# Performance work log

Hardware: AMD Instinct MI355X
Metric: run time of the kernel (lower is better)

The kernel has to match this reference:

```python
import jax, jax.numpy as jnp
import numpy as np

CHUNK = 32


def l2norm(x):
    return x * jax.lax.rsqrt(jnp.sum(x * x, -1, keepdims=True) + 1e-6)


def causal_dwconv(x, w):
    # x: (b, l, C), w: (C, 1, k) -- depthwise causal 1D conv (left pad k-1)
    k = w.shape[-1]
    xt = jnp.transpose(x, (0, 2, 1))
    xt = jnp.pad(xt, ((0, 0), (0, 0), (k - 1, 0)))
    y = jax.lax.conv_general_dilated(xt, w, (1,), 'VALID',
                                     dimension_numbers=('NCH', 'OIH', 'NCH'),
                                     feature_group_count=xt.shape[1])
    return jnp.transpose(y, (0, 2, 1))


def delta_rule_chunkwise(q, k, v, beta):
    # q,k: (b,h,L,dk), v: (b,h,L,dv), beta: (b,h,L). L must be divisible by CHUNK.
    b, h, L, dk = q.shape
    dv = v.shape[-1]
    n = L // CHUNK
    q = l2norm(q)
    k = l2norm(k)
    v = v * beta[..., None]
    kb = k * beta[..., None]
    resh = lambda t: t.reshape(b, h, n, CHUNK, t.shape[-1])
    q, k, v, kb = (resh(t) for t in (q, k, v, kb))
    strict = jnp.tril(jnp.ones((CHUNK, CHUNK), bool), -1)
    A = jnp.where(strict, -(kb @ jnp.swapaxes(k, -1, -2)), 0.0)
    eye = jnp.eye(CHUNK, dtype=A.dtype)
    # UT transform: the sequential forward-substitution loop computes T = (I - A)^{-1}
    T = jax.scipy.linalg.solve_triangular(eye - A, jnp.broadcast_to(eye, A.shape), lower=True)
    u = T @ v
    w = T @ kb
    incl = jnp.tril(jnp.ones((CHUNK, CHUNK), bool))  # lower incl. diag

    def step(S, xs):
        q_i, k_i, u_i, w_i = xs
        attn = jnp.where(incl, q_i @ jnp.swapaxes(k_i, -1, -2), 0.0)
        u_hat = u_i - w_i @ S
        o_i = q_i @ S + attn @ u_hat
        return S + jnp.swapaxes(k_i, -1, -2) @ u_hat, o_i

    xs = tuple(jnp.moveaxis(t, 2, 0) for t in (q, k, u, w))
    S0 = jnp.zeros((b, h, dk, dv), q.dtype)
    S, o = jax.lax.scan(step, S0, xs)
    o = jnp.moveaxis(o, 0, 2).reshape(b, h, L, dv)
    return o, S


def branch_stats(x):
    # per-head stats over the feature dim: mean, std(ddof=1), mean|x|, L2 norm
    m = jnp.mean(x, -1, keepdims=True)
    s = jnp.std(x, -1, keepdims=True, ddof=1)
    a = jnp.mean(jnp.abs(x), -1, keepdims=True)
    l = jnp.sqrt(jnp.sum(x * x, -1, keepdims=True))
    return jnp.concatenate([m, s, a, l], -1)


def reference(hidden_states, q_w, k_w, v_w, b_w, qc_w, kc_w, vc_w,
              fir_w1, fir_w3, fir_w7, fir_w31,
              mlp_w1, mlp_b1, mlp_w2, mlp_b2, gate_log_temp, onorm_w, o_w):
    B, L, D = hidden_states.shape
    H = gate_log_temp.shape[0]
    dk = q_w.shape[1] // H
    dv = v_w.shape[1] // H
    # projections + causal short conv + silu
    q = jax.nn.silu(causal_dwconv(hidden_states @ q_w, qc_w))
    k = jax.nn.silu(causal_dwconv(hidden_states @ k_w, kc_w))
    v = jax.nn.silu(causal_dwconv(hidden_states @ v_w, vc_w))
    q = q.reshape(B, L, H, dk)
    k = k.reshape(B, L, H, dk)
    v_direct = v.reshape(B, L, H, dv)
    beta = jax.nn.sigmoid(hidden_states @ b_w)  # (B,L,H)
    delta_out, _ = delta_rule_chunkwise(
        jnp.transpose(q, (0, 2, 1, 3)), jnp.transpose(k, (0, 2, 1, 3)),
        jnp.transpose(v_direct, (0, 2, 1, 3)), jnp.transpose(beta, (0, 2, 1)))
    delta_out = jnp.transpose(delta_out, (0, 2, 1, 3))  # (B,L,H,dv)
    # multi-scale depthwise FIR branches on v
    v_flat = v_direct.reshape(B, L, H * dv)
    firs = [causal_dwconv(v_flat, w).reshape(B, L, H, dv)
            for w in (fir_w1, fir_w3, fir_w7, fir_w31)]
    branches = firs + [delta_out, v_direct]  # num_streams = 6
    S = len(branches)
    stats = jnp.concatenate([branch_stats(x) for x in branches], -1)  # (B,L,H,S*4)
    gate_in = jnp.concatenate([hidden_states, stats.reshape(B, L, H * S * 4)], -1)
    hgate = jax.nn.gelu(gate_in @ mlp_w1 + mlp_b1, approximate=False)
    logits = (hgate @ mlp_w2 + mlp_b2).reshape(B, L, H, S)
    temp = jax.nn.softplus(gate_log_temp) + 0.5  # min_gate_temp = 0.5
    weights = jax.nn.softmax(logits / temp[None, None, :, None], axis=-1)
    fused = sum(weights[..., i, None] * br for i, br in enumerate(branches))
    # RMSNorm over head_v_dim (eps=1e-5)
    fused = fused * jax.lax.rsqrt(jnp.mean(fused * fused, -1, keepdims=True) + 1e-5) * onorm_w
    return fused.reshape(B, L, H * dv) @ o_w


def setup_inputs() -> dict:
    key = jax.random.key(0)
    B, L, D, H = 2, 2048, 1024, 4
    dk = dv = D // H
    S = 6
    ks = iter(jax.random.split(key, 32))
    nrm = lambda shape, s=0.02: jax.random.normal(next(ks), shape, jnp.float32) * s

    def fir(kw):
        # delta init (last tap = 1) plus small noise
        base = jnp.zeros((H * dv, 1, kw), jnp.float32).at[:, 0, -1].set(1.0)
        return base + nrm((H * dv, 1, kw))

    gate_in_dim = D + S * 4 * H  # 1120
    hgd = D * 2 // 2             # 1024
    b2 = np.zeros(H * S, np.float32)
    for h in range(H):
        b2[h * S + S - 1] = 2.0  # value_bias_init on direct-value stream
    return {
        'hidden_states': jax.random.normal(next(ks), (B, L, D), jnp.float32),
        'q_w': nrm((D, D)), 'k_w': nrm((D, D)), 'v_w': nrm((D, D)),
        'b_w': nrm((D, H)),
        'qc_w': nrm((D, 1, 4), 0.3), 'kc_w': nrm((D, 1, 4), 0.3), 'vc_w': nrm((D, 1, 4), 0.3),
        'fir_w1': fir(1), 'fir_w3': fir(3), 'fir_w7': fir(7), 'fir_w31': fir(31),
        'mlp_w1': nrm((gate_in_dim, hgd)), 'mlp_b1': jnp.zeros((hgd,), jnp.float32),
        'mlp_w2': nrm((hgd, H * S)), 'mlp_b2': jnp.asarray(b2),
        'gate_log_temp': jnp.zeros((H,), jnp.float32),
        'onorm_w': jnp.ones((dv,), jnp.float32),
        'o_w': nrm((D, D)),
    }
```

## Files before the change

kernel.cpp:

```cpp
#include <hip/hip_runtime.h>
#include <hip/hip_bf16.h>
#include <math.h>

#define B_ 2
#define L_ 2048
#define D_ 1024
#define H_ 4
#define NC 64

typedef unsigned short ushort_t;
typedef __bf16 bf16x8 __attribute__((ext_vector_type(8)));
typedef float f32x4 __attribute__((ext_vector_type(4)));
typedef ushort_t u16x8 __attribute__((ext_vector_type(8)));

__device__ __forceinline__ ushort_t f2bs(float f) {
    __hip_bfloat16 h = __float2bfloat16(f);
    ushort_t u;
    __builtin_memcpy(&u, &h, 2);
    return u;
}

__device__ __forceinline__ float wred(float v) {
    v += __shfl_down(v, 32);
    v += __shfl_down(v, 16);
    v += __shfl_down(v, 8);
    v += __shfl_down(v, 4);
    v += __shfl_down(v, 2);
    v += __shfl_down(v, 1);
    return v;
}

__device__ __forceinline__ void gload16(const void* g, void* l) {
    __builtin_amdgcn_global_load_lds((const __attribute__((address_space(1))) void*)g,
                                     (__attribute__((address_space(3))) void*)l, 16, 0, 0);
}

#define LGKM0_BAR()                                          \
    do {                                                     \
        asm volatile("s_waitcnt lgkmcnt(0)" ::: "memory");   \
        __builtin_amdgcn_s_barrier();                        \
    } while (0)

__global__ __launch_bounds__(256) void tcast_k(const float* __restrict__ W,
                                               ushort_t* __restrict__ WT, int K, int N) {
    __shared__ float tile[32 * 33];
    const int k0 = blockIdx.y << 5, n0 = blockIdx.x << 5;
    for (int e = threadIdx.x; e < 1024; e += 256)
        tile[(e >> 5) * 33 + (e & 31)] = W[(size_t)(k0 + (e >> 5)) * N + n0 + (e & 31)];
    __syncthreads();
    for (int e = threadIdx.x; e < 1024; e += 256)
        WT[(size_t)(n0 + (e >> 5)) * K + k0 + (e & 31)] = f2bs(tile[(e & 31) * 33 + (e >> 5)]);
}

__global__ __launch_bounds__(256) void cast_k(const float* __restrict__ x,
                                              ushort_t* __restrict__ y) {
    const int i = blockIdx.x * 256 + threadIdx.x;
    const float4 v = *(const float4*)&x[(size_t)i * 4];
    ushort4 p;
    p.x = f2bs(v.x); p.y = f2bs(v.y); p.z = f2bs(v.z); p.w = f2bs(v.w);
    *(ushort4*)&y[(size_t)i * 4] = p;
}

template <int ACT>
__global__ __launch_bounds__(256) void gemm_bf(const ushort_t* __restrict__ A,
                                               const ushort_t* __restrict__ Bt,
                                               const float* __restrict__ bias,
                                               float* __restrict__ C,
                                               int M, int N, int K) {
    __shared__ ushort_t As[128 * 32];
    __shared__ ushort_t Bs[128 * 32];
    const int t = threadIdx.x;
    const int wv = t >> 6, l = t & 63;
    const int m0 = blockIdx.y << 7, n0 = blockIdx.x << 7;
    const int wm = wv & 1, wn = wv >> 1;
    const int q4 = l >> 4, c16 = l & 15;
    f32x4 acc[4][4];
#pragma unroll
    for (int i = 0; i < 4; ++i)
#pragma unroll
        for (int j = 0; j < 4; ++j) {
            f32x4 z = {0.f, 0.f, 0.f, 0.f};
            acc[i][j] = z;
        }
    const int srow = (l >> 2);
    const int scol = (l & 3) << 3;
    for (int k0 = 0; k0 < K; k0 += 32) {
        __syncthreads();
#pragma unroll
        for (int si = 0; si < 2; ++si) {
            const int s = wv * 2 + si;
            gload16(&A[(size_t)(m0 + s * 16 + srow) * K + k0 + scol], &As[s * 512]);
            gload16(&Bt[(size_t)(n0 + s * 16 + srow) * K + k0 + scol], &Bs[s * 512]);
        }
        __syncthreads();
        bf16x8 af[4], bff[4];
#pragma unroll
        for (int mi = 0; mi < 4; ++mi)
            af[mi] = *(const bf16x8*)&As[(wm * 64 + mi * 16 + c16) * 32 + q4 * 8];
#pragma unroll
        for (int ni = 0; ni < 4; ++ni)
            bff[ni] = *(const bf16x8*)&Bs[(wn * 64 + ni * 16 + c16) * 32 + q4 * 8];
#pragma unroll
        for (int mi = 0; mi < 4; ++mi)
#pragma unroll
            for (int ni = 0; ni < 4; ++ni)
                acc[mi][ni] = __builtin_amdgcn_mfma_f32_16x16x32_bf16(af[mi], bff[ni],
                                                                     acc[mi][ni], 0, 0, 0);
    }
#pragma unroll
    for (int mi = 0; mi < 4; ++mi)
#pragma unroll
        for (int ni = 0; ni < 4; ++ni)
#pragma unroll
            for (int r = 0; r < 4; ++r) {
                const int row = m0 + wm * 64 + mi * 16 + q4 * 4 + r;
                const int col = n0 + wn * 64 + ni * 16 + c16;
                float v = acc[mi][ni][r];
                if (ACT == 1) {
                    v += bias[col];
                    v = 0.5f * v * (1.0f + erff(v * 0.70710678118654752f));
                }
                C[(size_t)row * N + col] = v;
            }
}

template <int DO_NORM, int EMIT_F32, int EMIT_BF>
__global__ __launch_bounds__(256) void convql_k(const float* __restrict__ X,
                                                const float* __restrict__ cw,
                                                float* __restrict__ Y,
                                                ushort_t* __restrict__ Ybf) {
    __shared__ float xs[35 * 256];
    const int bid = blockIdx.x;
    const int h = bid & 3, lt = (bid >> 2) & 63, b = bid >> 8;
    const int t = threadIdx.x;
    const int l0 = lt << 5;
    const int cg = (h << 8) | t;
    for (int e = t; e < 35 * 256; e += 256) {
        const int r = e >> 8, c = e & 255;
        const int gl = l0 + r - 3;
        xs[e] = (gl >= 0) ? X[((size_t)(b * L_) + gl) * 3072 + (h << 8) + c] : 0.f;
    }
    const float w0 = cw[cg * 4 + 0], w1 = cw[cg * 4 + 1];
    const float w2 = cw[cg * 4 + 2], w3 = cw[cg * 4 + 3];
    __syncthreads();
    float yr[32];
#pragma unroll
    for (int l = 0; l < 32; ++l) {
        const float a = xs[(l + 0) * 256 + t] * w0 + xs[(l + 1) * 256 + t] * w1 +
                        xs[(l + 2) * 256 + t] * w2 + xs[(l + 3) * 256 + t] * w3;
        yr[l] = a / (1.f + expf(-a));
    }
    if (DO_NORM) {
        __syncthreads();
#pragma unroll
        for (int l = 0; l < 32; ++l) xs[l * 256 + t] = yr[l];
        __syncthreads();
        const int wv = t >> 6, lane = t & 63;
#pragma unroll
        for (int ri = 0; ri < 8; ++ri) {
            const int r = wv * 8 + ri;
            float4 v = *(float4*)&xs[r * 256 + lane * 4];
            float ss = v.x * v.x + v.y * v.y + v.z * v.z + v.w * v.w;
            ss = wred(ss);
            ss = __shfl(ss, 0);
            const float s = rsqrtf(ss + 1e-6f);
            v.x *= s; v.y *= s; v.z *= s; v.w *= s;
            const size_t go = ((size_t)(b * L_) + l0 + r) * 1024 + (h << 8) + lane * 4;
            if (EMIT_F32) *(float4*)&Y[go] = v;
            if (EMIT_BF) {
                ushort4 p;
                p.x = f2bs(v.x); p.y = f2bs(v.y); p.z = f2bs(v.z); p.w = f2bs(v.w);
                *(ushort4*)&Ybf[go] = p;
            }
        }
    } else {
#pragma unroll
        for (int l = 0; l < 32; ++l)
            if (EMIT_F32) Y[((size_t)(b * L_) + l0 + l) * 1024 + cg] = yr[l];
    }
}

__global__ __launch_bounds__(256) void fir_k(const float* __restrict__ V,
                                             const float* __restrict__ w1w,
                                             const float* __restrict__ w3w,
                                             const float* __restrict__ w7w,
                                             const float* __restrict__ w31w,
                                             float* __restrict__ o1,
                                             float* __restrict__ o3,
                                             float* __restrict__ o7,
                                             float* __restrict__ o31) {
    __shared__ float xs[62 * 256];
    const int bid = blockIdx.x;
    const int h = bid & 3, lt = (bid >> 2) & 63, b = bid >> 8;
    const int t = threadIdx.x;
    const int l0 = lt << 5;
    const int cg = (h << 8) | t;
    for (int e = t; e < 62 * 256; e += 256) {
        const int r = e >> 8, c = e & 255;
        const int gl = l0 + r - 30;
        xs[e] = (gl >= 0) ? V[((size_t)(b * L_) + gl) * 1024 + (h << 8) + c] : 0.f;
    }
    float lw31[31], lw7[7], lw3[3];
#pragma unroll
    for (int j = 0; j < 31; ++j) lw31[j] = w31w[cg * 31 + j];
#pragma unroll
    for (int j = 0; j < 7; ++j) lw7[j] = w7w[cg * 7 + j];
#pragma unroll
    for (int j = 0; j < 3; ++j) lw3[j] = w3w[cg * 3 + j];
    const float lw1 = w1w[cg];
    __syncthreads();
    for (int l = 0; l < 32; ++l) {
        float a31 = 0.f, a7 = 0.f, a3 = 0.f, v = 0.f;
#pragma unroll
        for (int j = 0; j < 31; ++j) {
            v = xs[(l + j) * 256 + t];
            a31 += v * lw31[j];
            if (j >= 24) a7 += v * lw7[j - 24];
            if (j >= 28) a3 += v * lw3[j - 28];
        }
        const size_t go = ((size_t)(b * L_) + l0 + l) * 1024 + cg;
        o31[go] = a31;
        o7[go] = a7;
        o3[go] = a3;
        o1[go] = v * lw1;
    }
}

__global__ __launch_bounds__(64) void beta_k(const float* __restrict__ hs,
                                             const float* __restrict__ bw,
                                             float* __restrict__ beta,
                                             ushort_t* __restrict__ gin) {
    const int row = blockIdx.x;
    const int lane = threadIdx.x;
    float a0 = 0, a1 = 0, a2 = 0, a3 = 0;
    const float* hp = hs + (size_t)row * D_;
    ushort_t* gp = gin + (size_t)row * 1120;
    for (int c = lane; c < D_; c += 64) {
        const float x = hp[c];
        gp[c] = f2bs(x);
        a0 += x * bw[c * 4 + 0];
        a1 += x * bw[c * 4 + 1];
        a2 += x * bw[c * 4 + 2];
        a3 += x * bw[c * 4 + 3];
    }
    a0 = wred(a0); a1 = wred(a1); a2 = wred(a2); a3 = wred(a3);
    if (lane == 0) {
        float* o = beta + (size_t)row * 4;
        o[0] = 1.f / (1.f + expf(-a0));
        o[1] = 1.f / (1.f + expf(-a1));
        o[2] = 1.f / (1.f + expf(-a2));
        o[3] = 1.f / (1.f + expf(-a3));
    }
}

__global__ __launch_bounds__(256) void prep2_k(const ushort_t* __restrict__ qbf,
                                               const ushort_t* __restrict__ kbf,
                                               const float* __restrict__ vg,
                                               const float* __restrict__ beta,
                                               ushort_t* __restrict__ wbf,
                                               float* __restrict__ ub,
                                               ushort_t* __restrict__ atg,
                                               ushort_t* __restrict__ ktg) {
    __shared__ ushort_t k_lds[32 * 264];
    __shared__ ushort_t kT_lds[256 * 32];
    __shared__ ushort_t vT_lds[256 * 32];
    __shared__ float Am[32 * 33];
    __shared__ float Tm[32 * 33];
    __shared__ ushort_t Tb[32 * 40];
    __shared__ float beta_s[32];
    const int bid = blockIdx.x;
    const int bh = bid >> 6, ci = bid & 63;
    const int b = bh >> 2, h = bh & 3;
    const int t = threadIdx.x;
    const int wv = t >> 6, lane = t & 63;
    const int l16 = lane & 15, quad = lane >> 4;
    const size_t cb = (size_t)bid;
    const size_t grow = ((size_t)(b * L_ + ci * 32)) * 1024 + (h << 8);
    const f32x4 z4 = {0.f, 0.f, 0.f, 0.f};

    if (t < 32) beta_s[t] = beta[(size_t)(b * L_ + ci * 32 + t) * 4 + h];
#pragma unroll
    for (int j = 0; j < 4; ++j) {
        const int idx = j * 2048 + t * 8, r = idx >> 8, c = idx & 255;
        *(u16x8*)&k_lds[r * 264 + c] = *(const u16x8*)&kbf[grow + (size_t)r * 1024 + c];
    }
#pragma unroll
    for (int j = 0; j < 8; ++j) {
        const int e = j * 1024 + t * 4, r = e >> 8, c = e & 255;
        const float4 v4 = *(const float4*)&vg[grow + (size_t)r * 1024 + c];
        const float vv[4] = {v4.x, v4.y, v4.z, v4.w};
#pragma unroll
        for (int x = 0; x < 4; ++x) {
            const int cc = c + x;
            const int sp = (r >> 3) ^ ((cc >> 1) & 3);
            vT_lds[cc * 32 + sp * 8 + (r & 7)] = f2bs(vv[x]);
        }
    }
    const int mi = wv & 1, ni = wv >> 1;
    f32x4 g = z4, atv = z4;
#pragma unroll
    for (int s = 0; s < 8; ++s) {
        const bf16x8 a =
            *(const bf16x8*)&kbf[grow + (size_t)(mi * 16 + l16) * 1024 + s * 32 + (quad << 3)];
        const bf16x8 bb =
            *(const bf16x8*)&kbf[grow + (size_t)(ni * 16 + l16) * 1024 + s * 32 + (quad << 3)];
        const bf16x8 qa =
            *(const bf16x8*)&qbf[grow + (size_t)(mi * 16 + l16) * 1024 + s * 32 + (quad << 3)];
        g = __builtin_amdgcn_mfma_f32_16x16x32_bf16(a, bb, g, 0, 0, 0);
        atv = __builtin_amdgcn_mfma_f32_16x16x32_bf16(qa, bb, atv, 0, 0, 0);
    }
    __syncthreads();
#pragma unroll
    for (int r = 0; r < 4; ++r) {
        const int row = mi * 16 + (quad << 2) + r;
        const int col = ni * 16 + l16;
        Am[row * 33 + col] = (col < row) ? -beta_s[row] * g[r] : 0.f;
        Tm[row * 33 + col] = (row == col) ? 1.f : 0.f;
        atg[cb * 1024 + row * 32 + col] = (col <= row) ? f2bs(atv[r]) : (ushort_t)0;
    }
#pragma unroll
    for (int j = 0; j < 8; ++j) {
        const int e = j * 1024 + t * 4, r = e >> 8, c = e & 255;
#pragma unroll
        for (int x = 0; x < 4; ++x) {
            const int cc = c + x;
            const int sp = (r >> 3) ^ ((cc >> 1) & 3);
            kT_lds[cc * 32 + sp * 8 + (r & 7)] = k_lds[r * 264 + cc];
        }
    }
    __syncthreads();
    for (int i = 1; i < 32; ++i) {
        if (t < 32) {
            float s = 0.f;
            for (int j = 0; j < i; ++j) s += Am[i * 33 + j] * Tm[j * 33 + t];
            Tm[i * 33 + t] += s;
        }
        __syncthreads();
    }
#pragma unroll
    for (int j = 0; j < 4; ++j) {
        const int e = j * 256 + t, i = e >> 5, jj = e & 31;
        Tb[i * 40 + jj] = f2bs(Tm[i * 33 + jj] * beta_s[jj]);
    }
    __syncthreads();
    const bf16x8 tf = *(const bf16x8*)&Tb[(mi * 16 + l16) * 40 + (quad << 3)];
#pragma unroll
    for (int j = 0; j < 8; ++j) {
        const int nt = ni * 8 + j;
        const int d = (nt << 4) + l16;
        const int sp = quad ^ ((d >> 1) & 3);
        const bf16x8 kb = *(const bf16x8*)&kT_lds[d * 32 + (sp << 3)];
        const bf16x8 vb = *(const bf16x8*)&vT_lds[d * 32 + (sp << 3)];
        const f32x4 wacc = __builtin_amdgcn_mfma_f32_16x16x32_bf16(tf, kb, z4, 0, 0, 0);
        const f32x4 uacc = __builtin_amdgcn_mfma_f32_16x16x32_bf16(tf, vb, z4, 0, 0, 0);
#pragma unroll
        for (int r = 0; r < 4; ++r) {
            const int row = mi * 16 + (quad << 2) + r;
            wbf[cb * 8192 + row * 256 + d] = f2bs(wacc[r]);
            ub[cb * 8192 + (size_t)row * 256 + d] = uacc[r];
        }
    }
#pragma unroll
    for (int j = 0; j < 4; ++j) {
        const int idx = j * 2048 + t * 8;
        const int c = idx >> 5, sl = (idx & 31) >> 3;
        const int sp = sl ^ ((c >> 1) & 3);
        *(u16x8*)&ktg[cb * 8192 + c * 32 + sl * 8] = *(const u16x8*)&kT_lds[c * 32 + sp * 8];
    }
}

__global__ __launch_bounds__(256, 1) void scan4_k(const ushort_t* __restrict__ qbf,
                                                  const ushort_t* __restrict__ wbf,
                                                  const float* __restrict__ ubuf,
                                                  const ushort_t* __restrict__ atg,
                                                  const ushort_t* __restrict__ ktg,
                                                  float* __restrict__ dlt) {
    __shared__ ushort_t uh_lds[16 * 40];
    __shared__ ushort_t S_lds[16 * 264];
    const int t = threadIdx.x;
    const int wv = t >> 6, lane = t & 63;
    const int bh = blockIdx.x & 7, tile = blockIdx.x >> 3;
    const int b = bh >> 2, h = bh & 3;
    const int l16 = lane & 15, quad = lane >> 4;
    for (int e = t; e < 16 * 264; e += 256) S_lds[e] = 0;

    f32x4 Sacc[8];
#pragma unroll
    for (int j = 0; j < 8; ++j) {
        f32x4 z = {0.f, 0.f, 0.f, 0.f};
        Sacc[j] = z;
    }

    bf16x8 wfA[8], qfA[8], atfA, ktA[8];
    bf16x8 wfB[8], qfB[8], atfB, ktB[8];
    float uvA[4], uvB[4];

    auto loadf = [&](int ci, bf16x8* wf, bf16x8* qf, bf16x8& atf, float* uv, bf16x8* ktf) {
        const size_t cb = (size_t)(bh * NC + ci);
        if (wv < 2) {
            const ushort_t* wsrc = wbf + cb * 8192;
            const ushort_t* qsrc = qbf + ((size_t)(b * L_ + ci * 32)) * 1024 + (h << 8);
            const int i = (wv << 4) + l16;
#pragma unroll
            for (int s = 0; s < 8; ++s) {
                wf[s] = *(const bf16x8*)&wsrc[i * 256 + s * 32 + (quad << 3)];
                qf[s] = *(const bf16x8*)&qsrc[(size_t)i * 1024 + s * 32 + (quad << 3)];
            }
            atf = *(const bf16x8*)&atg[cb * 1024 + i * 32 + (quad << 3)];
#pragma unroll
            for (int r = 0; r < 4; ++r)
                uv[r] = ubuf[cb * 8192 + (size_t)((wv << 4) + (quad << 2) + r) * 256 +
                             (tile << 4) + l16];
        } else {
            const ushort_t* ksrc = ktg + cb * 8192;
#pragma unroll
            for (int j = 0; j < 8; ++j) {
                const int c = ((((wv - 2) << 3) + j) << 4) + l16;
                ktf[j] = *(const bf16x8*)&ksrc[c * 32 + (quad << 3)];
            }
        }
    };
    auto sfrag = [&](int k0) -> bf16x8 {
        return *(const bf16x8*)&S_lds[l16 * 264 + k0 + (quad << 3)];
    };
    auto uhfrag = [&]() -> bf16x8 {
        return *(const bf16x8*)&uh_lds[l16 * 40 + (quad << 3)];
    };
    auto compute = [&](int ci, bf16x8* wf, bf16x8* qf, bf16x8& atf, float* uv, bf16x8* ktf) {
        const size_t gbase = ((size_t)(b * L_ + ci * 32)) * D_ + (h << 8);
        if (wv < 2) {
            f32x4 acc = {0.f, 0.f, 0.f, 0.f};
#pragma unroll
            for (int s = 0; s < 8; ++s)
                acc = __builtin_amdgcn_mfma_f32_16x16x32_bf16(wf[s], sfrag(s * 32), acc, 0, 0, 0);
            ushort4 up;
            up.x = f2bs(uv[0] - acc[0]);
            up.y = f2bs(uv[1] - acc[1]);
            up.z = f2bs(uv[2] - acc[2]);
            up.w = f2bs(uv[3] - acc[3]);
            *(ushort4*)&uh_lds[l16 * 40 + (wv << 4) + (quad << 2)] = up;
        }
        LGKM0_BAR();
        if (wv < 2) {
            f32x4 o = {0.f, 0.f, 0.f, 0.f};
#pragma unroll
            for (int s = 0; s < 8; ++s)
                o = __builtin_amdgcn_mfma_f32_16x16x32_bf16(qf[s], sfrag(s * 32), o, 0, 0, 0);
            o = __builtin_amdgcn_mfma_f32_16x16x32_bf16(atf, uhfrag(), o, 0, 0, 0);
#pragma unroll
            for (int r = 0; r < 4; ++r)
                dlt[gbase + (size_t)((wv << 4) + (quad << 2) + r) * D_ + (tile << 4) + l16] =
                    o[r];
        } else {
            const bf16x8 uf = uhfrag();
#pragma unroll
            for (int j = 0; j < 8; ++j)
                Sacc[j] = __builtin_amdgcn_mfma_f32_16x16x32_bf16(ktf[j], uf, Sacc[j], 0, 0, 0);
        }
        LGKM0_BAR();
        if (wv >= 2) {
#pragma unroll
            for (int j = 0; j < 8; ++j) {
                const int c0 = ((((wv - 2) << 3) + j) << 4) + (quad << 2);
#pragma unroll
                for (int r = 0; r < 4; ++r)
                    S_lds[l16 * 264 + c0 + r] = f2bs(Sacc[j][r]);
            }
        }
        LGKM0_BAR();
    };

    loadf(0, wfA, qfA, atfA, uvA, ktA);
    LGKM0_BAR();
    for (int ci = 0; ci < NC; ci += 2) {
        loadf(ci + 1, wfB, qfB, atfB, uvB, ktB);
        compute(ci, wfA, qfA, atfA, uvA, ktA);
        if (ci + 2 < NC) loadf(ci + 2, wfA, qfA, atfA, uvA, ktA);
        compute(ci + 1, wfB, qfB, atfB, uvB, ktB);
    }
}

__global__ __launch_bounds__(64) void stats_k(const float* __restrict__ f1,
                                              const float* __restrict__ f3,
                                              const float* __restrict__ f7,
                                              const float* __restrict__ f31,
                                              const float* __restrict__ dl,
                                              const float* __restrict__ vv,
                                              ushort_t* __restrict__ gin) {
    const int row = blockIdx.x;
    const int lane = threadIdx.x;
    const float* ptrs[6] = {f1, f3, f7, f31, dl, vv};
    const size_t base = (size_t)row * 256;
    ushort_t* gp = gin + (size_t)(row >> 2) * 1120 + 1024 + (row & 3) * 24;
    for (int br = 0; br < 6; ++br) {
        const float4 x = *(const float4*)&ptrs[br][base + lane * 4];
        float s1 = x.x + x.y + x.z + x.w;
        float s2 = x.x * x.x + x.y * x.y + x.z * x.z + x.w * x.w;
        float sa = fabsf(x.x) + fabsf(x.y) + fabsf(x.z) + fabsf(x.w);
        s1 = wred(s1); s2 = wred(s2); sa = wred(sa);
        if (lane == 0) {
            const float m = s1 / 256.f;
            float var = (s2 - 256.f * m * m) / 255.f;
            if (var < 0.f) var = 0.f;
            gp[br * 4 + 0] = f2bs(m);
            gp[br * 4 + 1] = f2bs(sqrtf(var));
            gp[br * 4 + 2] = f2bs(sa / 256.f);
            gp[br * 4 + 3] = f2bs(sqrtf(s2));
        }
    }
}

__global__ __launch_bounds__(256) void wts_k(const float* __restrict__ hg,
                                             const float* __restrict__ w2,
                                             const float* __restrict__ b2,
                                             const float* __restrict__ glt,
                                             float* __restrict__ wts) {
    const int row = blockIdx.x;
    const int h = threadIdx.x >> 6, lane = threadIdx.x & 63;
    float hv[16];
    const float* hp = hg + (size_t)row * 1024;
#pragma unroll
    for (int ii = 0; ii < 16; ++ii) hv[ii] = hp[lane + 64 * ii];
    float lg[6];
#pragma unroll
    for (int s = 0; s < 6; ++s) {
        const int j = h * 6 + s;
        float acc = 0.f;
#pragma unroll
        for (int ii = 0; ii < 16; ++ii) acc += hv[ii] * w2[(size_t)(lane + 64 * ii) * 24 + j];
        lg[s] = wred(acc);
    }
    if (lane == 0) {
        const float temp = log1pf(expf(glt[h])) + 0.5f;
        float mx = -1e30f;
#pragma unroll
        for (int s = 0; s < 6; ++s) {
            lg[s] = (lg[s] + b2[h * 6 + s]) / temp;
            mx = fmaxf(mx, lg[s]);
        }
        float se = 0.f;
#pragma unroll
        for (int s = 0; s < 6; ++s) {
            lg[s] = expf(lg[s] - mx);
            se += lg[s];
        }
        float* o = &wts[(size_t)row * 24 + h * 6];
        const float inv = 1.f / se;
#pragma unroll
        for (int s = 0; s < 6; ++s) o[s] = lg[s] * inv;
    }
}

__global__ __launch_bounds__(1024) void fuse_k(const float* __restrict__ f1,
                                               const float* __restrict__ f3,
                                               const float* __restrict__ f7,
                                               const float* __restrict__ f31,
                                               const float* __restrict__ dl,
                                               const float* __restrict__ vv,
                                               const float* __restrict__ wts,
                                               const float* __restrict__ onw,
                                               ushort_t* __restrict__ fused) {
    __shared__ float wloc[24];
    __shared__ float psum[16];
    const int row = blockIdx.x, t = threadIdx.x;
    if (t < 24) wloc[t] = wts[(size_t)row * 24 + t];
    __syncthreads();
    const int h = t >> 8, dd = t & 255;
    const size_t idx = (size_t)row * 1024 + t;
    const float* ptrs[6] = {f1, f3, f7, f31, dl, vv};
    float f = 0.f;
#pragma unroll
    for (int br = 0; br < 6; ++br) f += wloc[h * 6 + br] * ptrs[br][idx];
    float ss = wred(f * f);
    const int wave = t >> 6;
    if ((t & 63) == 0) psum[wave] = ss;
    __syncthreads();
    const float tot = psum[h * 4 + 0] + psum[h * 4 + 1] + psum[h * 4 + 2] + psum[h * 4 + 3];
    const float scale = rsqrtf(tot / 256.f + 1e-5f);
    fused[idx] = f2bs(f * scale * onw[dd]);
}

extern "C" void kernel_launch(void* const* d_in, const int* in_sizes, int n_in,
                              void* d_out, int out_size, void* d_ws, size_t ws_size,
                              hipStream_t stream) {
    const float* hs   = (const float*)d_in[0];
    const float* q_w  = (const float*)d_in[1];
    const float* k_w  = (const float*)d_in[2];
    const float* v_w  = (const float*)d_in[3];
    const float* b_w  = (const float*)d_in[4];
    const float* qc_w = (const float*)d_in[5];
    const float* kc_w = (const float*)d_in[6];
    const float* vc_w = (const float*)d_in[7];
    const float* f1w  = (const float*)d_in[8];
    const float* f3w  = (const float*)d_in[9];
    const float* f7w  = (const float*)d_in[10];
    const float* f31w = (const float*)d_in[11];
    const float* w1   = (const float*)d_in[12];
    const float* b1   = (const float*)d_in[13];
    const float* w2   = (const float*)d_in[14];
    const float* b2   = (const float*)d_in[15];
    const float* glt  = (const float*)d_in[16];
    const float* onw  = (const float*)d_in[17];
    const float* o_w  = (const float*)d_in[18];
    float* out = (float*)d_out;

    const size_t SZ = (size_t)B_ * L_ * D_;
    float* qlin = (float*)d_ws;
    float* klin = qlin + SZ;
    float* vlin = klin + SZ;
    float* qbuf = vlin + SZ;
    float* kbuf = qbuf + SZ;
    float* vbuf = kbuf + SZ;
    float* f31b = vbuf + SZ;
    float* wb   = f31b + SZ;
    float* ub   = wb + SZ;
    float* dlt  = ub + SZ;
    float* beta = dlt + SZ;
    float* attn = beta + (size_t)B_ * L_ * H_;
    float* stat = attn + (size_t)B_ * H_ * NC * 1024;
    float* wts  = stat + (size_t)B_ * L_ * H_ * 24;
    float* f1b = qlin;
    float* f3b = klin;
    float* f7b = vlin;
    float* hgate = kbuf;
    float* qkv = qlin;

    ushort_t* hs_bf = (ushort_t*)dlt;
    ushort_t* qwT = (ushort_t*)f31b;
    ushort_t* kwT = (ushort_t*)f31b + 1048576;
    ushort_t* vwT = (ushort_t*)f31b + 2097152;
    ushort_t* qbf = (ushort_t*)f31b + 3145728;
    ushort_t* kbf = (ushort_t*)kbuf;
    ushort_t* gin_bf = (ushort_t*)qbuf;
    ushort_t* w1T = (ushort_t*)(wb + 2359296);
    ushort_t* owT = (ushort_t*)ub;
    ushort_t* fused_bf = (ushort_t*)kbuf;
    ushort_t* ktg = (ushort_t*)klin;
    ushort_t* wbf = (ushort_t*)wb;
    ushort_t* at_bf = (ushort_t*)attn;
    (void)stat;

    const int M = B_ * L_;

    tcast_k<<<dim3(32, 32), 256, 0, stream>>>(q_w, qwT, 1024, 1024);
    tcast_k<<<dim3(32, 32), 256, 0, stream>>>(k_w, kwT, 1024, 1024);
    tcast_k<<<dim3(32, 32), 256, 0, stream>>>(v_w, vwT, 1024, 1024);
    cast_k<<<4096, 256, 0, stream>>>(hs, hs_bf);
    gemm_bf<0><<<dim3(24, 32), 256, 0, stream>>>(hs_bf, qwT, nullptr, qkv, M, 3072, 1024);
    beta_k<<<M, 64, 0, stream>>>(hs, b_w, beta, gin_bf);
    convql_k<1, 0, 1><<<512, 256, 0, stream>>>(qkv + 0,    qc_w, nullptr, qbf);
    convql_k<1, 0, 1><<<512, 256, 0, stream>>>(qkv + 1024, kc_w, nullptr, kbf);
    convql_k<0, 1, 0><<<512, 256, 0, stream>>>(qkv + 2048, vc_w, vbuf, nullptr);
    prep2_k<<<B_ * H_ * NC, 256, 0, stream>>>(qbf, kbf, vbuf, beta, wbf, ub, at_bf, ktg);
    scan4_k<<<128, 256, 0, stream>>>(qbf, wbf, ub, at_bf, ktg, dlt);
    fir_k<<<512, 256, 0, stream>>>(vbuf, f1w, f3w, f7w, f31w, f1b, f3b, f7b, f31b);
    stats_k<<<M * H_, 64, 0, stream>>>(f1b, f3b, f7b, f31b, dlt, vbuf, gin_bf);
    tcast_k<<<dim3(32, 35), 256, 0, stream>>>(w1, w1T, 1120, 1024);
    gemm_bf<1><<<dim3(8, 32), 256, 0, stream>>>(gin_bf, w1T, b1, hgate, M, 1024, 1120);
    wts_k<<<M, 256, 0, stream>>>(hgate, w2, b2, glt, wts);
    fuse_k<<<M, 1024, 0, stream>>>(f1b, f3b, f7b, f31b, dlt, vbuf, wts, onw, fused_bf);
    tcast_k<<<dim3(32, 32), 256, 0, stream>>>(o_w, owT, 1024, 1024);
    gemm_bf<0><<<dim3(8, 32), 256, 0, stream>>>(fused_bf, owT, nullptr, out, M, 1024, 1024);
}
```

Baseline: 591.6 us.

## Store scan operands in MFMA fragment order and double-buffer S in LDS

```diff
diff --git a/kernel.cpp b/kernel.cpp
--- a/kernel.cpp
+++ b/kernel.cpp
@@ -257,22 +257,25 @@
                                                const ushort_t* __restrict__ kbf,
                                                const float* __restrict__ vg,
                                                const float* __restrict__ beta,
-                                               ushort_t* __restrict__ wbf,
-                                               float* __restrict__ ub,
-                                               ushort_t* __restrict__ atg,
-                                               ushort_t* __restrict__ ktg) {
+                                               ushort_t* __restrict__ qfr,
+                                               ushort_t* __restrict__ wfr,
+                                               float* __restrict__ ufr,
+                                               ushort_t* __restrict__ atfr,
+                                               ushort_t* __restrict__ ktfr) {
     __shared__ ushort_t k_lds[32 * 264];
     __shared__ ushort_t kT_lds[256 * 32];
     __shared__ ushort_t vT_lds[256 * 32];
     __shared__ float Am[32 * 33];
     __shared__ float Tm[32 * 33];
     __shared__ ushort_t Tb[32 * 40];
+    __shared__ ushort_t at_s[32 * 40];
     __shared__ float beta_s[32];
     const int bid = blockIdx.x;
     const int bh = bid >> 6, ci = bid & 63;
     const int b = bh >> 2, h = bh & 3;
     const int t = threadIdx.x;
     const int wv = t >> 6, lane = t & 63;
+    const int mi = wv & 1, ni = wv >> 1;
     const int l16 = lane & 15, quad = lane >> 4;
     const size_t cb = (size_t)bid;
     const size_t grow = ((size_t)(b * L_ + ci * 32)) * 1024 + (h << 8);
@@ -296,7 +299,6 @@
             vT_lds[cc * 32 + sp * 8 + (r & 7)] = f2bs(vv[x]);
         }
     }
-    const int mi = wv & 1, ni = wv >> 1;
     f32x4 g = z4, atv = z4;
 #pragma unroll
     for (int s = 0; s < 8; ++s) {
@@ -308,6 +310,7 @@
             *(const bf16x8*)&qbf[grow + (size_t)(mi * 16 + l16) * 1024 + s * 32 + (quad << 3)];
         g = __builtin_amdgcn_mfma_f32_16x16x32_bf16(a, bb, g, 0, 0, 0);
         atv = __builtin_amdgcn_mfma_f32_16x16x32_bf16(qa, bb, atv, 0, 0, 0);
+        if (ni == 0) *(bf16x8*)&qfr[((cb * 2 + mi) * 8 + s) * 512 + lane * 8] = qa;
     }
     __syncthreads();
 #pragma unroll
@@ -316,7 +319,7 @@
         const int col = ni * 16 + l16;
         Am[row * 33 + col] = (col < row) ? -beta_s[row] * g[r] : 0.f;
         Tm[row * 33 + col] = (row == col) ? 1.f : 0.f;
-        atg[cb * 1024 + row * 32 + col] = (col <= row) ? f2bs(atv[r]) : (ushort_t)0;
+        at_s[row * 40 + col] = (col <= row) ? f2bs(atv[r]) : (ushort_t)0;
     }
 #pragma unroll
     for (int j = 0; j < 8; ++j) {
@@ -329,6 +332,17 @@
         }
     }
     __syncthreads();
+    if (wv < 2) {
+        const u16x8 av = *(const u16x8*)&at_s[(wv * 16 + l16) * 40 + (quad << 3)];
+        *(u16x8*)&atfr[(cb * 2 + wv) * 512 + lane * 8] = av;
+    }
+#pragma unroll
+    for (int j2 = 0; j2 < 4; ++j2) {
+        const int tc = wv * 4 + j2;
+        const int c = tc * 16 + l16;
+        const int sp = quad ^ ((c >> 1) & 3);
+        *(u16x8*)&ktfr[(cb * 16 + tc) * 512 + lane * 8] = *(const u16x8*)&kT_lds[c * 32 + sp * 8];
+    }
     for (int i = 1; i < 32; ++i) {
         if (t < 32) {
             float s = 0.f;
@@ -353,36 +367,38 @@
         const bf16x8 vb = *(const bf16x8*)&vT_lds[d * 32 + (sp << 3)];
         const f32x4 wacc = __builtin_amdgcn_mfma_f32_16x16x32_bf16(tf, kb, z4, 0, 0, 0);
         const f32x4 uacc = __builtin_amdgcn_mfma_f32_16x16x32_bf16(tf, vb, z4, 0, 0, 0);
+        *(float4*)&ufr[((cb * 16 + nt) * 2 + mi) * 256 + lane * 4] =
+            make_float4(uacc[0], uacc[1], uacc[2], uacc[3]);
 #pragma unroll
         for (int r = 0; r < 4; ++r) {
             const int row = mi * 16 + (quad << 2) + r;
-            wbf[cb * 8192 + row * 256 + d] = f2bs(wacc[r]);
-            ub[cb * 8192 + (size_t)row * 256 + d] = uacc[r];
-        }
-    }
-#pragma unroll
-    for (int j = 0; j < 4; ++j) {
-        const int idx = j * 2048 + t * 8;
-        const int c = idx >> 5, sl = (idx & 31) >> 3;
-        const int sp = sl ^ ((c >> 1) & 3);
-        *(u16x8*)&ktg[cb * 8192 + c * 32 + sl * 8] = *(const u16x8*)&kT_lds[c * 32 + sp * 8];
-    }
-}
-
-__global__ __launch_bounds__(256, 1) void scan4_k(const ushort_t* __restrict__ qbf,
-                                                  const ushort_t* __restrict__ wbf,
-                                                  const float* __restrict__ ubuf,
-                                                  const ushort_t* __restrict__ atg,
-                                                  const ushort_t* __restrict__ ktg,
+            k_lds[row * 264 + d] = f2bs(wacc[r]);
+        }
+    }
+    __syncthreads();
+    if (wv < 2) {
+#pragma unroll
+        for (int s = 0; s < 8; ++s) {
+            const u16x8 wv8 = *(const u16x8*)&k_lds[(wv * 16 + l16) * 264 + s * 32 + (quad << 3)];
+            *(u16x8*)&wfr[((cb * 2 + wv) * 8 + s) * 512 + lane * 8] = wv8;
+        }
+    }
+}
+
+__global__ __launch_bounds__(256, 1) void scan5_k(const ushort_t* __restrict__ qfr,
+                                                  const ushort_t* __restrict__ wfr,
+                                                  const float* __restrict__ ufr,
+                                                  const ushort_t* __restrict__ atfr,
+                                                  const ushort_t* __restrict__ ktfr,
                                                   float* __restrict__ dlt) {
     __shared__ ushort_t uh_lds[16 * 40];
-    __shared__ ushort_t S_lds[16 * 264];
+    __shared__ ushort_t S_lds[2][16 * 264];
     const int t = threadIdx.x;
     const int wv = t >> 6, lane = t & 63;
     const int bh = blockIdx.x & 7, tile = blockIdx.x >> 3;
     const int b = bh >> 2, h = bh & 3;
     const int l16 = lane & 15, quad = lane >> 4;
-    for (int e = t; e < 16 * 264; e += 256) S_lds[e] = 0;
+    for (int e = t; e < 16 * 264; e += 256) S_lds[0][e] = 0;
 
     f32x4 Sacc[8];
 #pragma unroll
@@ -398,73 +414,77 @@
     auto loadf = [&](int ci, bf16x8* wf, bf16x8* qf, bf16x8& atf, float* uv, bf16x8* ktf) {
         const size_t cb = (size_t)(bh * NC + ci);
         if (wv < 2) {
-            const ushort_t* wsrc = wbf + cb * 8192;
-            const ushort_t* qsrc = qbf + ((size_t)(b * L_ + ci * 32)) * 1024 + (h << 8);
-            const int i = (wv << 4) + l16;
+            const ushort_t* wsrc = wfr + (cb * 2 + wv) * 8 * 512;
+            const ushort_t* qsrc = qfr + (cb * 2 + wv) * 8 * 512;
 #pragma unroll
             for (int s = 0; s < 8; ++s) {
-                wf[s] = *(const bf16x8*)&wsrc[i * 256 + s * 32 + (quad << 3)];
-                qf[s] = *(const bf16x8*)&qsrc[(size_t)i * 1024 + s * 32 + (quad << 3)];
+                wf[s] = *(const bf16x8*)&wsrc[s * 512 + lane * 8];
+                qf[s] = *(const bf16x8*)&qsrc[s * 512 + lane * 8];
             }
-            atf = *(const bf16x8*)&atg[cb * 1024 + i * 32 + (quad << 3)];
-#pragma unroll
-            for (int r = 0; r < 4; ++r)
-                uv[r] = ubuf[cb * 8192 + (size_t)((wv << 4) + (quad << 2) + r) * 256 +
-                             (tile << 4) + l16];
+            atf = *(const bf16x8*)&atfr[(cb * 2 + wv) * 512 + lane * 8];
+            const float4 u4 = *(const float4*)&ufr[((cb * 16 + tile) * 2 + wv) * 256 + lane * 4];
+            uv[0] = u4.x; uv[1] = u4.y; uv[2] = u4.z; uv[3] = u4.w;
         } else {
-            const ushort_t* ksrc = ktg + cb * 8192;
+            const ushort_t* ksrc = ktfr + cb * 16 * 512;
 #pragma unroll
             for (int j = 0; j < 8; ++j) {
-                const int c = ((((wv - 2) << 3) + j) << 4) + l16;
-                ktf[j] = *(const bf16x8*)&ksrc[c * 32 + (quad << 3)];
+                const int tc = ((wv - 2) << 3) + j;
+                ktf[j] = *(const bf16x8*)&ksrc[tc * 512 + lane * 8];
             }
         }
     };
-    auto sfrag = [&](int k0) -> bf16x8 {
-        return *(const bf16x8*)&S_lds[l16 * 264 + k0 + (quad << 3)];
+    auto sfrag = [&](int p, int k0) -> bf16x8 {
+        return *(const bf16x8*)&S_lds[p][l16 * 264 + k0 + (quad << 3)];
     };
     auto uhfrag = [&]() -> bf16x8 {
         return *(const bf16x8*)&uh_lds[l16 * 40 + (quad << 3)];
     };
     auto compute = [&](int ci, bf16x8* wf, bf16x8* qf, bf16x8& atf, float* uv, bf16x8* ktf) {
+        const int p = ci & 1;
         const size_t gbase = ((size_t)(b * L_ + ci * 32)) * D_ + (h << 8);
         if (wv < 2) {
-            f32x4 acc = {0.f, 0.f, 0.f, 0.f};
-#pragma unroll
-            for (int s = 0; s < 8; ++s)
-                acc = __builtin_amdgcn_mfma_f32_16x16x32_bf16(wf[s], sfrag(s * 32), acc, 0, 0, 0);
+            f32x4 a0 = {0.f, 0.f, 0.f, 0.f}, a1 = {0.f, 0.f, 0.f, 0.f};
+#pragma unroll
+            for (int s = 0; s < 8; s += 2) {
+                a0 = __builtin_amdgcn_mfma_f32_16x16x32_bf16(wf[s], sfrag(p, s * 32), a0, 0, 0, 0);
+                a1 = __builtin_amdgcn_mfma_f32_16x16x32_bf16(wf[s + 1], sfrag(p, s * 32 + 32), a1,
+                                                             0, 0, 0);
+            }
             ushort4 up;
-            up.x = f2bs(uv[0] - acc[0]);
-            up.y = f2bs(uv[1] - acc[1]);
-            up.z = f2bs(uv[2] - acc[2]);
-            up.w = f2bs(uv[3] - acc[3]);
+            up.x = f2bs(uv[0] - a0[0] - a1[0]);
+            up.y = f2bs(uv[1] - a0[1] - a1[1]);
+            up.z = f2bs(uv[2] - a0[2] - a1[2]);
+            up.w = f2bs(uv[3] - a0[3] - a1[3]);
             *(ushort4*)&uh_lds[l16 * 40 + (wv << 4) + (quad << 2)] = up;
         }
         LGKM0_BAR();
         if (wv < 2) {
-            f32x4 o = {0.f, 0.f, 0.f, 0.f};
-#pragma unroll
-            for (int s = 0; s < 8; ++s)
-                o = __builtin_amdgcn_mfma_f32_16x16x32_bf16(qf[s], sfrag(s * 32), o, 0, 0, 0);
-            o = __builtin_amdgcn_mfma_f32_16x16x32_bf16(atf, uhfrag(), o, 0, 0, 0);
+            f32x4 o0 = {0.f, 0.f, 0.f, 0.f}, o1 = {0.f, 0.f, 0.f, 0.f};
+#pragma unroll
+            for (int s = 0; s < 8; s += 2) {
+                o0 = __builtin_amdgcn_mfma_f32_16x16x32_bf16(qf[s], sfrag(p, s * 32), o0, 0, 0, 0);
+                o1 = __builtin_amdgcn_mfma_f32_16x16x32_bf16(qf[s + 1], sfrag(p, s * 32 + 32), o1,
+                                                             0, 0, 0);
+            }
+            o0 = __builtin_amdgcn_mfma_f32_16x16x32_bf16(atf, uhfrag(), o0, 0, 0, 0);
 #pragma unroll
             for (int r = 0; r < 4; ++r)
                 dlt[gbase + (size_t)((wv << 4) + (quad << 2) + r) * D_ + (tile << 4) + l16] =
-                    o[r];
+                    o0[r] + o1[r];
         } else {
             const bf16x8 uf = uhfrag();
 #pragma unroll
             for (int j = 0; j < 8; ++j)
                 Sacc[j] = __builtin_amdgcn_mfma_f32_16x16x32_bf16(ktf[j], uf, Sacc[j], 0, 0, 0);
-        }
-        LGKM0_BAR();
-        if (wv >= 2) {
 #pragma unroll
             for (int j = 0; j < 8; ++j) {
                 const int c0 = ((((wv - 2) << 3) + j) << 4) + (quad << 2);
-#pragma unroll
-                for (int r = 0; r < 4; ++r)
-                    S_lds[l16 * 264 + c0 + r] = f2bs(Sacc[j][r]);
+                ushort4 pk;
+                pk.x = f2bs(Sacc[j][0]);
+                pk.y = f2bs(Sacc[j][1]);
+                pk.z = f2bs(Sacc[j][2]);
+                pk.w = f2bs(Sacc[j][3]);
+                *(ushort4*)&S_lds[p ^ 1][l16 * 264 + c0] = pk;
             }
         }
         LGKM0_BAR();
@@ -617,13 +637,12 @@
     float* dlt  = ub + SZ;
     float* beta = dlt + SZ;
     float* attn = beta + (size_t)B_ * L_ * H_;
-    float* stat = attn + (size_t)B_ * H_ * NC * 1024;
-    float* wts  = stat + (size_t)B_ * L_ * H_ * 24;
     float* f1b = qlin;
     float* f3b = klin;
     float* f7b = vlin;
     float* hgate = kbuf;
     float* qkv = qlin;
+    float* wts = attn + (size_t)B_ * H_ * NC * 1024;
 
     ushort_t* hs_bf = (ushort_t*)dlt;
     ushort_t* qwT = (ushort_t*)f31b;
@@ -635,10 +654,11 @@
     ushort_t* w1T = (ushort_t*)(wb + 2359296);
     ushort_t* owT = (ushort_t*)ub;
     ushort_t* fused_bf = (ushort_t*)kbuf;
-    ushort_t* ktg = (ushort_t*)klin;
-    ushort_t* wbf = (ushort_t*)wb;
-    ushort_t* at_bf = (ushort_t*)attn;
-    (void)stat;
+    ushort_t* ktfr = (ushort_t*)klin;
+    ushort_t* qfr = (ushort_t*)klin + SZ;
+    ushort_t* wfr = (ushort_t*)wb;
+    float* ufr = ub;
+    ushort_t* atfr = (ushort_t*)attn;
 
     const int M = B_ * L_;
 
@@ -651,8 +671,8 @@
     convql_k<1, 0, 1><<<512, 256, 0, stream>>>(qkv + 0,    qc_w, nullptr, qbf);
     convql_k<1, 0, 1><<<512, 256, 0, stream>>>(qkv + 1024, kc_w, nullptr, kbf);
     convql_k<0, 1, 0><<<512, 256, 0, stream>>>(qkv + 2048, vc_w, vbuf, nullptr);
-    prep2_k<<<B_ * H_ * NC, 256, 0, stream>>>(qbf, kbf, vbuf, beta, wbf, ub, at_bf, ktg);
-    scan4_k<<<128, 256, 0, stream>>>(qbf, wbf, ub, at_bf, ktg, dlt);
+    prep2_k<<<B_ * H_ * NC, 256, 0, stream>>>(qbf, kbf, vbuf, beta, qfr, wfr, ufr, atfr, ktfr);
+    scan5_k<<<128, 256, 0, stream>>>(qfr, wfr, ufr, atfr, ktfr, dlt);
     fir_k<<<512, 256, 0, stream>>>(vbuf, f1w, f3w, f7w, f31w, f1b, f3b, f7b, f31b);
     stats_k<<<M * H_, 64, 0, stream>>>(f1b, f3b, f7b, f31b, dlt, vbuf, gin_bf);
     tcast_k<<<dim3(32, 35), 256, 0, stream>>>(w1, w1T, 1120, 1024);
```

Measured after the change: 544.0 us. 1.09x faster.
